# Performance work log

Measured on AMD Instinct MI355X. Metric: run time of the kernel, lower is better.

Reference implementation:

```python
import jax, jax.numpy as jnp
import numpy as np

C = 128
NUM_HEADS = 4
WS = 4
LN_EPS = 1e-5


def setup_inputs() -> dict:
    key = jax.random.key(0)
    ks = jax.random.split(key, 8)
    x = jax.random.normal(ks[0], (2, C, 64, 64, 64), dtype=jnp.float32)
    s = 0.02
    return {
        "x": x,
        "ln_g": jnp.ones((C,), jnp.float32),
        "ln_b": jnp.zeros((C,), jnp.float32),
        "in_proj_w": jax.random.normal(ks[1], (3 * C, C), jnp.float32) * s,
        "in_proj_b": jnp.zeros((3 * C,), jnp.float32),
        "out_proj_w": jax.random.normal(ks[2], (C, C), jnp.float32) * s,
        "out_proj_b": jnp.zeros((C,), jnp.float32),
        "conv_w": jax.random.normal(ks[3], (C, C), jnp.float32) * s,  # 1x1x1 conv == pointwise linear
        "conv_b": jnp.zeros((C,), jnp.float32),
    }


def reference(x, ln_g, ln_b, in_proj_w, in_proj_b, out_proj_w, out_proj_b, conv_w, conv_b):
    B, Cc, D, H, W = x.shape
    ws = WS
    h = NUM_HEADS
    hd = Cc // h
    residual = x
    # D,H,W are multiples of ws so pad amounts are 0 (faithful to the (ws - dim % ws) % ws path)
    nD, nH, nW = D // ws, H // ws, W // ws
    # window partition: [B,C,D,H,W] -> [B*nWin, ws^3, C]
    xw = x.reshape(B, Cc, nD, ws, nH, ws, nW, ws)
    xw = xw.transpose(0, 2, 4, 6, 3, 5, 7, 1).reshape(B * nD * nH * nW, ws * ws * ws, Cc)
    # LayerNorm over channels
    mu = jnp.mean(xw, axis=-1, keepdims=True)
    var = jnp.var(xw, axis=-1, keepdims=True)
    xn = (xw - mu) * jax.lax.rsqrt(var + LN_EPS) * ln_g + ln_b
    # MHA (self-attention, batch_first): packed qkv projection
    qkv = jnp.einsum('ntc,oc->nto', xn, in_proj_w) + in_proj_b  # [N,T,3C]
    q, k, v = jnp.split(qkv, 3, axis=-1)
    N, T, _ = q.shape
    q = q.reshape(N, T, h, hd).transpose(0, 2, 1, 3)  # [N,h,T,hd]
    k = k.reshape(N, T, h, hd).transpose(0, 2, 1, 3)
    v = v.reshape(N, T, h, hd).transpose(0, 2, 1, 3)
    scores = jnp.einsum('nhqd,nhkd->nhqk', q, k) / jnp.sqrt(jnp.asarray(hd, q.dtype))
    attn = jax.nn.softmax(scores, axis=-1)
    o = jnp.einsum('nhqk,nhkd->nhqd', attn, v)  # [N,h,T,hd]
    o = o.transpose(0, 2, 1, 3).reshape(N, T, Cc)
    attn_out = jnp.einsum('ntc,oc->nto', o, out_proj_w) + out_proj_b
    xw = xw + attn_out
    # window merge: [B*nWin, ws^3, C] -> [B,C,D,H,W]
    y = xw.reshape(B, nD, nH, nW, ws, ws, ws, Cc)
    y = y.transpose(0, 7, 1, 4, 2, 5, 3, 6).reshape(B, Cc, D, H, W)
    # 1x1x1 conv projection + residual
    out = jnp.einsum('oc,bcdhw->bodhw', conv_w, y) + conv_b[None, :, None, None, None]
    return out + residual
```

## Files before the change

### kernel.cpp

```cpp
#include <hip/hip_runtime.h>

typedef unsigned short ushort_t;
typedef __attribute__((ext_vector_type(8))) short short8;
typedef __attribute__((ext_vector_type(4))) float f32x4;

#define LN_EPS 1e-5f

#define XW_OFF 0
#define XN_OFF 33792
#define Q_OFF  0
#define K_OFF  20480
#define V_OFF  40960
#define P_OFF  0
#define O_OFF  0
#define Y_OFF  17408
#define SMEM_BYTES 59392

static __device__ __forceinline__ ushort_t f2bf(float f) {
    union { float f; unsigned int u; } cv; cv.f = f;
    unsigned int x = cv.u + 0x7FFFu + ((cv.u >> 16) & 1u);
    return (ushort_t)(x >> 16);
}

static __device__ __forceinline__ short8 loadw8(const float* p) {
    float4 a = *(const float4*)p;
    float4 b = *(const float4*)(p + 4);
    short8 r;
    r[0] = (short)f2bf(a.x); r[1] = (short)f2bf(a.y); r[2] = (short)f2bf(a.z); r[3] = (short)f2bf(a.w);
    r[4] = (short)f2bf(b.x); r[5] = (short)f2bf(b.y); r[6] = (short)f2bf(b.z); r[7] = (short)f2bf(b.w);
    return r;
}

__global__ __launch_bounds__(512, 4) void wattn_kernel(
    const float* __restrict__ x,
    const float* __restrict__ ln_g,
    const float* __restrict__ ln_b,
    const float* __restrict__ w_qkv,
    const float* __restrict__ b_qkv,
    const float* __restrict__ w_out,
    const float* __restrict__ b_out,
    const float* __restrict__ w_cv,
    const float* __restrict__ b_cv,
    float* __restrict__ out)
{
    extern __shared__ char smem[];
    float*    xw  = (float*)(smem + XW_OFF);
    ushort_t* xn  = (ushort_t*)(smem + XN_OFF);
    ushort_t* qls = (ushort_t*)(smem + Q_OFF);
    ushort_t* kls = (ushort_t*)(smem + K_OFF);
    ushort_t* vls = (ushort_t*)(smem + V_OFF);
    ushort_t* pls = (ushort_t*)(smem + P_OFF);
    ushort_t* ols = (ushort_t*)(smem + O_OFF);
    ushort_t* yls = (ushort_t*)(smem + Y_OFF);

    const int tid  = threadIdx.x;
    const int lane = tid & 63;
    const int wv   = tid >> 6;
    const int l15  = lane & 15;
    const int quad = lane >> 4;

    const int win = (blockIdx.x & 7) * 1024 + (blockIdx.x >> 3);
    const int bN  = win >> 12;
    const int dz  = (win >> 8) & 15;
    const int hy  = (win >> 4) & 15;
    const int wx  = win & 15;
    const long base = ((long)(bN * 128) * 64 + dz * 4) * 4096 + (long)(hy * 4) * 64 + wx * 4;

    #pragma unroll
    for (int j = 0; j < 4; ++j) {
        int i  = tid + j * 512;
        int c  = i >> 4;
        int td = (i >> 2) & 3;
        int th = i & 3;
        float4 v = *(const float4*)(x + base + (long)c * 262144 + td * 4096 + th * 64);
        int t0 = td * 16 + th * 4;
        xw[(t0 + 0) * 132 + c] = v.x;
        xw[(t0 + 1) * 132 + c] = v.y;
        xw[(t0 + 2) * 132 + c] = v.z;
        xw[(t0 + 3) * 132 + c] = v.w;
    }
    __syncthreads();

    {
        int t = tid >> 3;
        int p = tid & 7;
        const float4* xp = (const float4*)(xw + t * 132 + p * 16);
        float4 v0 = xp[0], v1 = xp[1], v2 = xp[2], v3 = xp[3];
        float vals[16] = {v0.x,v0.y,v0.z,v0.w, v1.x,v1.y,v1.z,v1.w,
                          v2.x,v2.y,v2.z,v2.w, v3.x,v3.y,v3.z,v3.w};
        float s = 0.f, ss = 0.f;
        #pragma unroll
        for (int j = 0; j < 16; ++j) { s += vals[j]; ss += vals[j] * vals[j]; }
        #pragma unroll
        for (int off = 1; off < 8; off <<= 1) {
            s  += __shfl_xor(s, off, 64);
            ss += __shfl_xor(ss, off, 64);
        }
        float mu   = s * 0.0078125f;
        float var  = ss * 0.0078125f - mu * mu;
        float rstd = rsqrtf(var + LN_EPS);
        const float4* gp = (const float4*)(ln_g + p * 16);
        const float4* bp = (const float4*)(ln_b + p * 16);
        float4 g0 = gp[0], g1 = gp[1], g2 = gp[2], g3 = gp[3];
        float4 b0 = bp[0], b1 = bp[1], b2 = bp[2], b3 = bp[3];
        float gv[16] = {g0.x,g0.y,g0.z,g0.w, g1.x,g1.y,g1.z,g1.w,
                        g2.x,g2.y,g2.z,g2.w, g3.x,g3.y,g3.z,g3.w};
        float bv[16] = {b0.x,b0.y,b0.z,b0.w, b1.x,b1.y,b1.z,b1.w,
                        b2.x,b2.y,b2.z,b2.w, b3.x,b3.y,b3.z,b3.w};
        short8 o0, o1;
        #pragma unroll
        for (int j = 0; j < 8; ++j)  o0[j] = (short)f2bf((vals[j]     - mu) * rstd * gv[j]     + bv[j]);
        #pragma unroll
        for (int j = 0; j < 8; ++j)  o1[j] = (short)f2bf((vals[j + 8] - mu) * rstd * gv[j + 8] + bv[j + 8]);
        *(short8*)(xn + t * 136 + p * 16)     = o0;
        *(short8*)(xn + t * 136 + p * 16 + 8) = o1;
    }
    __syncthreads();

    {
        const int n_base = wv * 48;
        f32x4 acc[4][3];
        #pragma unroll
        for (int mi = 0; mi < 4; ++mi)
            #pragma unroll
            for (int ni = 0; ni < 3; ++ni) acc[mi][ni] = (f32x4){0.f, 0.f, 0.f, 0.f};
        #pragma unroll
        for (int ks = 0; ks < 4; ++ks) {
            int k0 = ks * 32 + quad * 8;
            short8 a[4], bfr[3];
            #pragma unroll
            for (int mi = 0; mi < 4; ++mi) a[mi] = *(const short8*)(xn + (mi * 16 + l15) * 136 + k0);
            #pragma unroll
            for (int ni = 0; ni < 3; ++ni) bfr[ni] = loadw8(w_qkv + (n_base + ni * 16 + l15) * 128 + k0);
            #pragma unroll
            for (int ni = 0; ni < 3; ++ni)
                #pragma unroll
                for (int mi = 0; mi < 4; ++mi)
                    acc[mi][ni] = __builtin_amdgcn_mfma_f32_16x16x32_bf16(a[mi], bfr[ni], acc[mi][ni], 0, 0, 0);
        }
        __syncthreads();
        #pragma unroll
        for (int ni = 0; ni < 3; ++ni) {
            int col  = n_base + ni * 16 + l15;
            float bias = b_qkv[col];
            int sect = col >> 7;
            int cc   = col & 127;
            int h = cc >> 5, d = cc & 31;
            #pragma unroll
            for (int mi = 0; mi < 4; ++mi)
                #pragma unroll
                for (int r = 0; r < 4; ++r) {
                    int row = mi * 16 + quad * 4 + r;
                    ushort_t val = f2bf(acc[mi][ni][r] + bias);
                    if (sect == 0)      qls[h * 2560 + row * 40 + d] = val;
                    else if (sect == 1) kls[h * 2560 + row * 40 + d] = val;
                    else                vls[h * 2304 + d * 72 + row] = val;
                }
        }
    }
    __syncthreads();

    {
        const int h  = wv >> 1;
        const int m0 = (wv & 1) * 32;
        const ushort_t* qh = qls + h * 2560;
        const ushort_t* kh = kls + h * 2560;
        f32x4 sc[2][4];
        #pragma unroll
        for (int mi = 0; mi < 2; ++mi)
            #pragma unroll
            for (int ni = 0; ni < 4; ++ni) sc[mi][ni] = (f32x4){0.f, 0.f, 0.f, 0.f};
        {
            int kq = quad * 8;
            short8 a[2], bfr[4];
            #pragma unroll
            for (int mi = 0; mi < 2; ++mi) a[mi] = *(const short8*)(qh + (m0 + mi * 16 + l15) * 40 + kq);
            #pragma unroll
            for (int ni = 0; ni < 4; ++ni) bfr[ni] = *(const short8*)(kh + (ni * 16 + l15) * 40 + kq);
            #pragma unroll
            for (int ni = 0; ni < 4; ++ni)
                #pragma unroll
                for (int mi = 0; mi < 2; ++mi)
                    sc[mi][ni] = __builtin_amdgcn_mfma_f32_16x16x32_bf16(a[mi], bfr[ni], sc[mi][ni], 0, 0, 0);
        }
        const float scale = 0.1767766952966369f;
        float pv[2][4][4];
        #pragma unroll
        for (int mi = 0; mi < 2; ++mi)
            #pragma unroll
            for (int r = 0; r < 4; ++r) {
                float v0 = sc[mi][0][r] * scale, v1 = sc[mi][1][r] * scale;
                float v2 = sc[mi][2][r] * scale, v3 = sc[mi][3][r] * scale;
                float mx = fmaxf(fmaxf(v0, v1), fmaxf(v2, v3));
                #pragma unroll
                for (int off = 1; off < 16; off <<= 1) mx = fmaxf(mx, __shfl_xor(mx, off, 64));
                float e0 = __expf(v0 - mx), e1 = __expf(v1 - mx), e2 = __expf(v2 - mx), e3 = __expf(v3 - mx);
                float sum = e0 + e1 + e2 + e3;
                #pragma unroll
                for (int off = 1; off < 16; off <<= 1) sum += __shfl_xor(sum, off, 64);
                float inv = 1.f / sum;
                pv[mi][0][r] = e0 * inv; pv[mi][1][r] = e1 * inv;
                pv[mi][2][r] = e2 * inv; pv[mi][3][r] = e3 * inv;
            }
        __syncthreads();
        ushort_t* ph = pls + h * 4608;
        #pragma unroll
        for (int mi = 0; mi < 2; ++mi)
            #pragma unroll
            for (int ni = 0; ni < 4; ++ni)
                #pragma unroll
                for (int r = 0; r < 4; ++r)
                    ph[(m0 + mi * 16 + quad * 4 + r) * 72 + ni * 16 + l15] = f2bf(pv[mi][ni][r]);
        __syncthreads();
        f32x4 oacc[2][2];
        #pragma unroll
        for (int mi = 0; mi < 2; ++mi)
            #pragma unroll
            for (int ni = 0; ni < 2; ++ni) oacc[mi][ni] = (f32x4){0.f, 0.f, 0.f, 0.f};
        #pragma unroll
        for (int kk = 0; kk < 2; ++kk) {
            int kq = kk * 32 + quad * 8;
            short8 a[2], bfr[2];
            #pragma unroll
            for (int mi = 0; mi < 2; ++mi) a[mi] = *(const short8*)(ph + (m0 + mi * 16 + l15) * 72 + kq);
            #pragma unroll
            for (int ni = 0; ni < 2; ++ni) bfr[ni] = *(const short8*)(vls + h * 2304 + (ni * 16 + l15) * 72 + kq);
            #pragma unroll
            for (int ni = 0; ni < 2; ++ni)
                #pragma unroll
                for (int mi = 0; mi < 2; ++mi)
                    oacc[mi][ni] = __builtin_amdgcn_mfma_f32_16x16x32_bf16(a[mi], bfr[ni], oacc[mi][ni], 0, 0, 0);
        }
        __syncthreads();
        #pragma unroll
        for (int mi = 0; mi < 2; ++mi)
            #pragma unroll
            for (int ni = 0; ni < 2; ++ni)
                #pragma unroll
                for (int r = 0; r < 4; ++r)
                    ols[(m0 + mi * 16 + quad * 4 + r) * 136 + h * 32 + ni * 16 + l15] = f2bf(oacc[mi][ni][r]);
    }
    __syncthreads();

    const int n0  = wv * 16;
    const int col = n0 + l15;
    float res[4][4];
    #pragma unroll
    for (int mi = 0; mi < 4; ++mi) {
        float4 r4 = *(const float4*)(x + base + (long)col * 262144 + mi * 4096 + quad * 64);
        res[mi][0] = r4.x; res[mi][1] = r4.y; res[mi][2] = r4.z; res[mi][3] = r4.w;
    }

    {
        f32x4 acc[4];
        #pragma unroll
        for (int mi = 0; mi < 4; ++mi) acc[mi] = (f32x4){0.f, 0.f, 0.f, 0.f};
        #pragma unroll
        for (int ks = 0; ks < 4; ++ks) {
            int k0 = ks * 32 + quad * 8;
            short8 bfr = loadw8(w_out + (n0 + l15) * 128 + k0);
            #pragma unroll
            for (int mi = 0; mi < 4; ++mi) {
                short8 a = *(const short8*)(ols + (mi * 16 + l15) * 136 + k0);
                acc[mi] = __builtin_amdgcn_mfma_f32_16x16x32_bf16(a, bfr, acc[mi], 0, 0, 0);
            }
        }
        float bias = b_out[col];
        #pragma unroll
        for (int mi = 0; mi < 4; ++mi)
            #pragma unroll
            for (int r = 0; r < 4; ++r) {
                int row = mi * 16 + quad * 4 + r;
                yls[row * 136 + col] = f2bf(acc[mi][r] + bias + res[mi][r]);
            }
    }
    __syncthreads();

    {
        f32x4 acc[4];
        #pragma unroll
        for (int mi = 0; mi < 4; ++mi) acc[mi] = (f32x4){0.f, 0.f, 0.f, 0.f};
        #pragma unroll
        for (int ks = 0; ks < 4; ++ks) {
            int k0 = ks * 32 + quad * 8;
            short8 bfr = loadw8(w_cv + (n0 + l15) * 128 + k0);
            #pragma unroll
            for (int mi = 0; mi < 4; ++mi) {
                short8 a = *(const short8*)(yls + (mi * 16 + l15) * 136 + k0);
                acc[mi] = __builtin_amdgcn_mfma_f32_16x16x32_bf16(a, bfr, acc[mi], 0, 0, 0);
            }
        }
        float bias = b_cv[col];
        #pragma unroll
        for (int mi = 0; mi < 4; ++mi) {
            float4 v;
            v.x = acc[mi][0] + bias + res[mi][0];
            v.y = acc[mi][1] + bias + res[mi][1];
            v.z = acc[mi][2] + bias + res[mi][2];
            v.w = acc[mi][3] + bias + res[mi][3];
            *(float4*)(out + base + (long)col * 262144 + mi * 4096 + quad * 64) = v;
        }
    }
}

extern "C" void kernel_launch(void* const* d_in, const int* in_sizes, int n_in,
                              void* d_out, int out_size, void* d_ws, size_t ws_size,
                              hipStream_t stream) {
    (void)in_sizes; (void)n_in; (void)d_ws; (void)ws_size; (void)out_size;
    wattn_kernel<<<dim3(8192), dim3(512), SMEM_BYTES, stream>>>(
        (const float*)d_in[0], (const float*)d_in[1], (const float*)d_in[2],
        (const float*)d_in[3], (const float*)d_in[4], (const float*)d_in[5],
        (const float*)d_in[6], (const float*)d_in[7], (const float*)d_in[8],
        (float*)d_out);
}
```

Before: 911.6 us.

## Pre-convert weights to bf16, swizzle LDS layouts, and shrink shared memory

```diff
diff --git a/kernel.cpp b/kernel.cpp
--- a/kernel.cpp
+++ b/kernel.cpp
@@ -2,6 +2,7 @@
 
 typedef unsigned short ushort_t;
 typedef __attribute__((ext_vector_type(8))) short short8;
+typedef __attribute__((ext_vector_type(4))) short s16x4;
 typedef __attribute__((ext_vector_type(4))) float f32x4;
 
 #define LN_EPS 1e-5f
@@ -9,12 +10,14 @@
 #define XW_OFF 0
 #define XN_OFF 33792
 #define Q_OFF  0
-#define K_OFF  20480
-#define V_OFF  40960
+#define K_OFF  16384
+#define V_OFF  32768
 #define P_OFF  0
 #define O_OFF  0
 #define Y_OFF  17408
-#define SMEM_BYTES 59392
+#define SMEM_BYTES 51200
+
+#define WS_NEED 163840
 
 static __device__ __forceinline__ ushort_t f2bf(float f) {
     union { float f; unsigned int u; } cv; cv.f = f;
@@ -31,7 +34,28 @@
     return r;
 }
 
-__global__ __launch_bounds__(512, 4) void wattn_kernel(
+static __device__ __forceinline__ int qk_i(int row, int d) {
+    return row * 32 + (d ^ ((row & 3) << 3));
+}
+static __device__ __forceinline__ int p_i(int row, int col) {
+    return row * 64 + (col ^ ((row & 7) << 3));
+}
+
+__global__ void wconv_kernel(const float* __restrict__ wq, const float* __restrict__ wo,
+                             const float* __restrict__ wc, ushort_t* __restrict__ ws) {
+    int i = blockIdx.x * 256 + threadIdx.x;
+    float4 v;
+    if (i < 12288)      v = ((const float4*)wq)[i];
+    else if (i < 16384) v = ((const float4*)wo)[i - 12288];
+    else                v = ((const float4*)wc)[i - 16384];
+    s16x4 s;
+    s[0] = (short)f2bf(v.x); s[1] = (short)f2bf(v.y);
+    s[2] = (short)f2bf(v.z); s[3] = (short)f2bf(v.w);
+    *(s16x4*)(ws + i * 4) = s;
+}
+
+template <bool PRE>
+__global__ __launch_bounds__(512, 6) void wattn_kernel(
     const float* __restrict__ x,
     const float* __restrict__ ln_g,
     const float* __restrict__ ln_b,
@@ -41,6 +65,7 @@
     const float* __restrict__ b_out,
     const float* __restrict__ w_cv,
     const float* __restrict__ b_cv,
+    const ushort_t* __restrict__ wbf,
     float* __restrict__ out)
 {
     extern __shared__ char smem[];
@@ -74,20 +99,25 @@
         int th = i & 3;
         float4 v = *(const float4*)(x + base + (long)c * 262144 + td * 4096 + th * 64);
         int t0 = td * 16 + th * 4;
-        xw[(t0 + 0) * 132 + c] = v.x;
-        xw[(t0 + 1) * 132 + c] = v.y;
-        xw[(t0 + 2) * 132 + c] = v.z;
-        xw[(t0 + 3) * 132 + c] = v.w;
+        int cs = c ^ ((th >> 1) << 2) ^ ((td & 1) << 3);
+        xw[(t0 + 0) * 132 + cs] = v.x;
+        xw[(t0 + 1) * 132 + cs] = v.y;
+        xw[(t0 + 2) * 132 + cs] = v.z;
+        xw[(t0 + 3) * 132 + cs] = v.w;
     }
     __syncthreads();
 
     {
         int t = tid >> 3;
         int p = tid & 7;
-        const float4* xp = (const float4*)(xw + t * 132 + p * 16);
-        float4 v0 = xp[0], v1 = xp[1], v2 = xp[2], v3 = xp[3];
-        float vals[16] = {v0.x,v0.y,v0.z,v0.w, v1.x,v1.y,v1.z,v1.w,
-                          v2.x,v2.y,v2.z,v2.w, v3.x,v3.y,v3.z,v3.w};
+        int sw = (((t >> 3) & 1) << 2) | (((t >> 4) & 1) << 3);
+        float vals[16];
+        #pragma unroll
+        for (int m = 0; m < 4; ++m) {
+            float4 v = *(const float4*)(xw + t * 132 + p * 16 + ((4 * m) ^ sw));
+            vals[4 * m + 0] = v.x; vals[4 * m + 1] = v.y;
+            vals[4 * m + 2] = v.z; vals[4 * m + 3] = v.w;
+        }
         float s = 0.f, ss = 0.f;
         #pragma unroll
         for (int j = 0; j < 16; ++j) { s += vals[j]; ss += vals[j] * vals[j]; }
@@ -131,7 +161,10 @@
             #pragma unroll
             for (int mi = 0; mi < 4; ++mi) a[mi] = *(const short8*)(xn + (mi * 16 + l15) * 136 + k0);
             #pragma unroll
-            for (int ni = 0; ni < 3; ++ni) bfr[ni] = loadw8(w_qkv + (n_base + ni * 16 + l15) * 128 + k0);
+            for (int ni = 0; ni < 3; ++ni) {
+                if constexpr (PRE) bfr[ni] = *(const short8*)(wbf + (n_base + ni * 16 + l15) * 128 + k0);
+                else               bfr[ni] = loadw8(w_qkv + (n_base + ni * 16 + l15) * 128 + k0);
+            }
             #pragma unroll
             for (int ni = 0; ni < 3; ++ni)
                 #pragma unroll
@@ -152,8 +185,8 @@
                 for (int r = 0; r < 4; ++r) {
                     int row = mi * 16 + quad * 4 + r;
                     ushort_t val = f2bf(acc[mi][ni][r] + bias);
-                    if (sect == 0)      qls[h * 2560 + row * 40 + d] = val;
-                    else if (sect == 1) kls[h * 2560 + row * 40 + d] = val;
+                    if (sect == 0)      qls[h * 2048 + qk_i(row, d)] = val;
+                    else if (sect == 1) kls[h * 2048 + qk_i(row, d)] = val;
                     else                vls[h * 2304 + d * 72 + row] = val;
                 }
         }
@@ -163,20 +196,19 @@
     {
         const int h  = wv >> 1;
         const int m0 = (wv & 1) * 32;
-        const ushort_t* qh = qls + h * 2560;
-        const ushort_t* kh = kls + h * 2560;
+        const ushort_t* qh = qls + h * 2048;
+        const ushort_t* kh = kls + h * 2048;
         f32x4 sc[2][4];
         #pragma unroll
         for (int mi = 0; mi < 2; ++mi)
             #pragma unroll
             for (int ni = 0; ni < 4; ++ni) sc[mi][ni] = (f32x4){0.f, 0.f, 0.f, 0.f};
         {
-            int kq = quad * 8;
             short8 a[2], bfr[4];
             #pragma unroll
-            for (int mi = 0; mi < 2; ++mi) a[mi] = *(const short8*)(qh + (m0 + mi * 16 + l15) * 40 + kq);
-            #pragma unroll
-            for (int ni = 0; ni < 4; ++ni) bfr[ni] = *(const short8*)(kh + (ni * 16 + l15) * 40 + kq);
+            for (int mi = 0; mi < 2; ++mi) a[mi] = *(const short8*)(qh + qk_i(m0 + mi * 16 + l15, quad * 8));
+            #pragma unroll
+            for (int ni = 0; ni < 4; ++ni) bfr[ni] = *(const short8*)(kh + qk_i(ni * 16 + l15, quad * 8));
             #pragma unroll
             for (int ni = 0; ni < 4; ++ni)
                 #pragma unroll
@@ -203,14 +235,14 @@
                 pv[mi][2][r] = e2 * inv; pv[mi][3][r] = e3 * inv;
             }
         __syncthreads();
-        ushort_t* ph = pls + h * 4608;
+        ushort_t* ph = pls + h * 4096;
         #pragma unroll
         for (int mi = 0; mi < 2; ++mi)
             #pragma unroll
             for (int ni = 0; ni < 4; ++ni)
                 #pragma unroll
                 for (int r = 0; r < 4; ++r)
-                    ph[(m0 + mi * 16 + quad * 4 + r) * 72 + ni * 16 + l15] = f2bf(pv[mi][ni][r]);
+                    ph[p_i(m0 + mi * 16 + quad * 4 + r, ni * 16 + l15)] = f2bf(pv[mi][ni][r]);
         __syncthreads();
         f32x4 oacc[2][2];
         #pragma unroll
@@ -222,7 +254,7 @@
             int kq = kk * 32 + quad * 8;
             short8 a[2], bfr[2];
             #pragma unroll
-            for (int mi = 0; mi < 2; ++mi) a[mi] = *(const short8*)(ph + (m0 + mi * 16 + l15) * 72 + kq);
+            for (int mi = 0; mi < 2; ++mi) a[mi] = *(const short8*)(ph + p_i(m0 + mi * 16 + l15, kq));
             #pragma unroll
             for (int ni = 0; ni < 2; ++ni) bfr[ni] = *(const short8*)(vls + h * 2304 + (ni * 16 + l15) * 72 + kq);
             #pragma unroll
@@ -258,7 +290,9 @@
         #pragma unroll
         for (int ks = 0; ks < 4; ++ks) {
             int k0 = ks * 32 + quad * 8;
-            short8 bfr = loadw8(w_out + (n0 + l15) * 128 + k0);
+            short8 bfr;
+            if constexpr (PRE) bfr = *(const short8*)(wbf + 49152 + (n0 + l15) * 128 + k0);
+            else               bfr = loadw8(w_out + (n0 + l15) * 128 + k0);
             #pragma unroll
             for (int mi = 0; mi < 4; ++mi) {
                 short8 a = *(const short8*)(ols + (mi * 16 + l15) * 136 + k0);
@@ -283,7 +317,9 @@
         #pragma unroll
         for (int ks = 0; ks < 4; ++ks) {
             int k0 = ks * 32 + quad * 8;
-            short8 bfr = loadw8(w_cv + (n0 + l15) * 128 + k0);
+            short8 bfr;
+            if constexpr (PRE) bfr = *(const short8*)(wbf + 65536 + (n0 + l15) * 128 + k0);
+            else               bfr = loadw8(w_cv + (n0 + l15) * 128 + k0);
             #pragma unroll
             for (int mi = 0; mi < 4; ++mi) {
                 short8 a = *(const short8*)(yls + (mi * 16 + l15) * 136 + k0);
@@ -306,10 +342,22 @@
 extern "C" void kernel_launch(void* const* d_in, const int* in_sizes, int n_in,
                               void* d_out, int out_size, void* d_ws, size_t ws_size,
                               hipStream_t stream) {
-    (void)in_sizes; (void)n_in; (void)d_ws; (void)ws_size; (void)out_size;
-    wattn_kernel<<<dim3(8192), dim3(512), SMEM_BYTES, stream>>>(
-        (const float*)d_in[0], (const float*)d_in[1], (const float*)d_in[2],
-        (const float*)d_in[3], (const float*)d_in[4], (const float*)d_in[5],
-        (const float*)d_in[6], (const float*)d_in[7], (const float*)d_in[8],
-        (float*)d_out);
-}
+    (void)in_sizes; (void)n_in; (void)out_size;
+    const float* x    = (const float*)d_in[0];
+    const float* ln_g = (const float*)d_in[1];
+    const float* ln_b = (const float*)d_in[2];
+    const float* wq   = (const float*)d_in[3];
+    const float* bq   = (const float*)d_in[4];
+    const float* wo   = (const float*)d_in[5];
+    const float* bo   = (const float*)d_in[6];
+    const float* wc   = (const float*)d_in[7];
+    const float* bc   = (const float*)d_in[8];
+    if (d_ws && ws_size >= WS_NEED) {
+        wconv_kernel<<<dim3(80), dim3(256), 0, stream>>>(wq, wo, wc, (ushort_t*)d_ws);
+        wattn_kernel<true><<<dim3(8192), dim3(512), SMEM_BYTES, stream>>>(
+            x, ln_g, ln_b, wq, bq, wo, bo, wc, bc, (const ushort_t*)d_ws, (float*)d_out);
+    } else {
+        wattn_kernel<false><<<dim3(8192), dim3(512), SMEM_BYTES, stream>>>(
+            x, ln_g, ln_b, wq, bq, wo, bo, wc, bc, nullptr, (float*)d_out);
+    }
+}
```

After: 923.5 us. Within noise of the previous version (+1.3%).
